# Kernel tuning notes

Hardware: AMD Instinct MI355X
Metric: run time of the kernel (lower is better)

## Reference

```python
import jax, jax.numpy as jnp
import numpy as np

B, T, D_MODEL, D_K = 4, 4096, 1024, 64

def setup_inputs() -> dict:
    key = jax.random.key(0)
    k1, k2, k3, k4, k5 = jax.random.split(key, 5)
    x = jax.random.normal(k1, (B, T, D_MODEL), dtype=jnp.float32)
    # rotary freqs_cis as (real, imag) pairs: unit-magnitude like real RoPE
    theta = 10000.0
    inv = 1.0 / (theta ** (jnp.arange(0, D_K, 2, dtype=jnp.float32) / D_K))  # [D_K//2]
    ang = jnp.arange(T, dtype=jnp.float32)[:, None] * inv[None, :]           # [T, D_K//2]
    freqs_cis = jnp.stack([jnp.cos(ang), jnp.sin(ang)], axis=-1)             # [T, D_K//2, 2]
    scale = 1.0 / np.sqrt(D_MODEL)
    Wq = jax.random.normal(k2, (D_MODEL, D_K), dtype=jnp.float32) * scale
    Wk = jax.random.normal(k3, (D_MODEL, D_K), dtype=jnp.float32) * scale
    Wv = jax.random.normal(k4, (D_MODEL, D_K), dtype=jnp.float32) * scale
    return {"x": x, "freqs_cis": freqs_cis, "Wq": Wq, "Wk": Wk, "Wv": Wv}

def _apply_rope(t, fr, fi):
    # t: [B,T,D_K]; fr/fi: [T, D_K//2]. Complex mult on (even, odd) pairs.
    tp = t.reshape(*t.shape[:-1], D_K // 2, 2)       # [B,T,P,2]
    tr, ti = tp[..., 0], tp[..., 1]
    or_ = tr * fr - ti * fi
    oi_ = tr * fi + ti * fr
    return jnp.stack([or_, oi_], axis=-1).reshape(*t.shape[:-1], D_K)

def reference(x, freqs_cis, Wq, Wk, Wv):
    q = x @ Wq                                       # [B,T,D_K]
    k = x @ Wk
    v = x @ Wv
    fr, fi = freqs_cis[..., 0], freqs_cis[..., 1]    # [T, D_K//2]
    q = _apply_rope(q, fr, fi)
    k = _apply_rope(k, fr, fi)
    wei = jnp.einsum('btd,bsd->bts', q, k) * (D_K ** -0.5)   # [B,T,T]
    causal = jnp.tril(jnp.ones((T, T), dtype=bool))
    wei = jnp.where(causal, wei, -jnp.inf)
    wei = jax.nn.softmax(wei, axis=-1)
    return jnp.einsum('bts,bsd->btd', wei, v)        # [B,T,D_K]
```

## Files before the change

### kernel.cpp

```cpp
#include <hip/hip_runtime.h>
#include <hip/hip_bf16.h>

#define BB 4
#define TT 4096
#define DM 1024
#define DK 64
#define NSPLIT 8

using f32x4  = __attribute__((ext_vector_type(4))) float;
using bf16x8 = __attribute__((ext_vector_type(8))) short;

__device__ __forceinline__ short f2bf(float f) {
    __hip_bfloat16 h = __float2bfloat16(f);
    return __builtin_bit_cast(short, h);
}
__device__ __forceinline__ float bf2f(short s) {
    unsigned int u = ((unsigned int)(unsigned short)s) << 16;
    return __builtin_bit_cast(float, u);
}

__global__ __launch_bounds__(256) void wt_kernel(const float* __restrict__ Wq,
                                                 const float* __restrict__ Wk,
                                                 const float* __restrict__ Wv,
                                                 short* __restrict__ Wt) {
    int idx = blockIdx.x * 256 + threadIdx.x;
    if (idx >= 192 * 1024) return;
    int n = idx >> 10;
    int m = idx & 1023;
    const float* W = (n < 64) ? Wq : (n < 128) ? Wk : Wv;
    int c = n & 63;
    Wt[idx] = f2bf(W[m * 64 + c]);
}

__global__ __launch_bounds__(256, 4) void proj_rope(const float* __restrict__ x,
                                                    const float* __restrict__ freqs,
                                                    const short* __restrict__ Wt,
                                                    short* __restrict__ q,
                                                    short* __restrict__ k,
                                                    short* __restrict__ vt)
{
    __shared__ short As[2][4096];
    __shared__ short Bs[2][4096];

    int t  = threadIdx.x;
    int w  = t >> 6;
    int l  = t & 63;
    int lr = l & 15;
    int lg = (l >> 4) & 3;
    int bx = blockIdx.x;
    int mt = (bx & 7) * 32 + (bx >> 3) / 3;
    int nh = (bx >> 3) % 3;
    int m0 = mt * 64;

    int arow = t >> 2;
    int au2  = (t & 3) * 2;
    int aswz = arow & 7;
    const float* gA = x  + (size_t)(m0 + arow) * DM + au2 * 8;
    const short* gB = Wt + (size_t)(nh * 64 + arow) * DM + au2 * 8;

    f32x4 ar[4]; bf16x8 br[2];

#define LOADG(c_) do { int kk = (c_) << 6;                     \
        ar[0] = *(const f32x4*)(gA + kk);                      \
        ar[1] = *(const f32x4*)(gA + kk + 4);                  \
        ar[2] = *(const f32x4*)(gA + kk + 8);                  \
        ar[3] = *(const f32x4*)(gA + kk + 12);                 \
        br[0] = *(const bf16x8*)(gB + kk);                     \
        br[1] = *(const bf16x8*)(gB + kk + 8);                 \
    } while (0)

#define WRITELDS(buf_) do {                                                    \
        int sa = arow * 64;                                                    \
        bf16x8 a0_, a1_;                                                       \
        for (int j_ = 0; j_ < 4; ++j_) {                                       \
            a0_[j_] = f2bf(ar[0][j_]); a0_[4 + j_] = f2bf(ar[1][j_]);          \
            a1_[j_] = f2bf(ar[2][j_]); a1_[4 + j_] = f2bf(ar[3][j_]);          \
        }                                                                      \
        *(bf16x8*)&As[buf_][sa + (((au2    ) ^ aswz) << 3)] = a0_;             \
        *(bf16x8*)&As[buf_][sa + (((au2 + 1) ^ aswz) << 3)] = a1_;             \
        *(bf16x8*)&Bs[buf_][sa + (((au2    ) ^ aswz) << 3)] = br[0];           \
        *(bf16x8*)&Bs[buf_][sa + (((au2 + 1) ^ aswz) << 3)] = br[1];           \
    } while (0)

    f32x4 acc[4];
#pragma unroll
    for (int i = 0; i < 4; ++i) acc[i] = (f32x4){0.f, 0.f, 0.f, 0.f};

    LOADG(0); WRITELDS(0); LOADG(1);
    __syncthreads();

    int cur = 0;
    int r7 = lr & 7;
    int amrow = (w * 16 + lr) * 64;
    for (int ch = 0; ch < 16; ++ch) {
#pragma unroll
        for (int s = 0; s < 2; ++s) {
            int u0 = s * 4 + lg;
            bf16x8 af = *(const bf16x8*)&As[cur][amrow + ((u0 ^ r7) << 3)];
#pragma unroll
            for (int nt = 0; nt < 4; ++nt) {
                bf16x8 bfr = *(const bf16x8*)&Bs[cur][(nt * 16 + lr) * 64 + ((u0 ^ r7) << 3)];
                acc[nt] = __builtin_amdgcn_mfma_f32_16x16x32_bf16(af, bfr, acc[nt], 0, 0, 0);
            }
        }
        if (ch + 1 < 16) {
            WRITELDS(cur ^ 1);
            if (ch + 2 < 16) LOADG(ch + 2);
            __syncthreads();
            cur ^= 1;
        }
    }
#undef LOADG
#undef WRITELDS

    __syncthreads();

    if (nh == 2) {
        short* vs = &Bs[0][0];
#pragma unroll
        for (int r = 0; r < 4; ++r)
#pragma unroll
            for (int nt = 0; nt < 4; ++nt)
                vs[(w * 16 + lg * 4 + r) * 64 + nt * 16 + lr] = f2bf(acc[nt][r]);
        __syncthreads();
        int b   = mt >> 6;
        int tt0 = (mt & 63) * 64;
        int c   = t >> 2;
        int toff = (t & 3) * 16;
        bf16x8 v0, v1;
#pragma unroll
        for (int j = 0; j < 8; ++j) {
            v0[j] = vs[(toff + j) * 64 + c];
            v1[j] = vs[(toff + 8 + j) * 64 + c];
        }
        short* dstv = vt + ((size_t)b * DK + c) * TT + tt0 + toff;
        *(bf16x8*)dstv = v0;
        *(bf16x8*)(dstv + 8) = v1;
    } else {
        short* dst = nh ? k : q;
        float postscale = nh ? 1.0f : 0.125f;
#pragma unroll
        for (int r = 0; r < 4; ++r) {
            int tg = m0 + w * 16 + lg * 4 + r;
            int tt = tg & (TT - 1);
#pragma unroll
            for (int nt = 0; nt < 4; ++nt) {
                int c = nt * 16 + lr;
                float e = acc[nt][r];
                float p = __shfl_xor(e, 1);
                float2 f = ((const float2*)freqs)[(size_t)tt * 32 + (c >> 1)];
                float sgn = (c & 1) ? f.y : -f.y;
                dst[(size_t)tg * DK + c] = f2bf((e * f.x + p * sgn) * postscale);
            }
        }
    }
}

__global__ __launch_bounds__(256, 4) void attn_kernel(const short* __restrict__ q,
                                                      const short* __restrict__ k,
                                                      const short* __restrict__ vt,
                                                      short* __restrict__ po,
                                                      float* __restrict__ ml)
{
    __shared__ short Kb[64][64];
    __shared__ short Vb[64][64];
    __shared__ short pbuf[4][16][72];

    int w  = threadIdx.x >> 6;
    int l  = threadIdx.x & 63;
    int lr = l & 15;
    int lg = l >> 4;
    int b  = blockIdx.y;
    int s  = blockIdx.z;
    int qt = 63 - blockIdx.x;
    int q0 = qt * 64;
    int qrow_wave = q0 + w * 16;

    const short* qB = q  + (size_t)b * TT * DK;
    const short* kB = k  + (size_t)b * TT * DK;
    const short* vB = vt + (size_t)b * DK * TT;

    bf16x8 qf0 = *(const bf16x8*)(qB + (size_t)(qrow_wave + lr) * DK + 8 * lg);
    bf16x8 qf1 = *(const bf16x8*)(qB + (size_t)(qrow_wave + lr) * DK + 32 + 8 * lg);

    f32x4 of[4];
#pragma unroll
    for (int i = 0; i < 4; ++i) of[i] = (f32x4){0.f, 0.f, 0.f, 0.f};
    float m[4], lsum[4];
#pragma unroll
    for (int r = 0; r < 4; ++r) { m[r] = -INFINITY; lsum[r] = 0.f; }

    int nt = (qt >= s) ? ((qt - s + NSPLIT) >> 3) : 0;

    int srow = threadIdx.x >> 2;
    int u0   = (threadIdx.x & 3) * 2;
    int p0s  = ((u0) ^ (srow & 7)) * 8;
    int p1s  = ((u0 + 1) ^ (srow & 7)) * 8;

    bf16x8 kr0, kr1, vr0, vr1;
    short* mypb = &pbuf[w][0][0];

#define ISSUE(tile_) do {                                                        \
        int kv0_ = (tile_) << 6;                                                 \
        const short* gk_ = kB + (size_t)(kv0_ + srow) * DK + (u0 * 8);           \
        const short* gv_ = vB + (size_t)srow * TT + kv0_ + (u0 * 8);             \
        kr0 = *(const bf16x8*)gk_; kr1 = *(const bf16x8*)(gk_ + 8);              \
        vr0 = *(const bf16x8*)gv_; vr1 = *(const bf16x8*)(gv_ + 8);              \
    } while (0)

#define WRITE() do {                                                             \
        *(bf16x8*)&Kb[srow][p0s] = kr0;                                         \
        *(bf16x8*)&Kb[srow][p1s] = kr1;                                         \
        *(bf16x8*)&Vb[srow][p0s] = vr0;                                         \
        *(bf16x8*)&Vb[srow][p1s] = vr1;                                         \
    } while (0)

    if (nt > 0) {
        ISSUE(s); WRITE();
        if (nt > 1) ISSUE(s + NSPLIT);
        __syncthreads();
        for (int i = 0; i < nt; ++i) {
            int kv0 = (s + i * NSPLIT) << 6;

            f32x4 sc[4];
#pragma unroll
            for (int c = 0; c < 4; ++c) sc[c] = (f32x4){0.f, 0.f, 0.f, 0.f};
#pragma unroll
            for (int c = 0; c < 4; ++c) {
                int row = c * 16 + lr;
                bf16x8 kf0 = *(const bf16x8*)&Kb[row][((lg) ^ (row & 7)) * 8];
                bf16x8 kf1 = *(const bf16x8*)&Kb[row][((4 + lg) ^ (row & 7)) * 8];
                sc[c] = __builtin_amdgcn_mfma_f32_16x16x32_bf16(qf0, kf0, sc[c], 0, 0, 0);
                sc[c] = __builtin_amdgcn_mfma_f32_16x16x32_bf16(qf1, kf1, sc[c], 0, 0, 0);
            }

            if (kv0 == q0) {
#pragma unroll
                for (int r = 0; r < 4; ++r) {
                    int qg = qrow_wave + lg * 4 + r;
#pragma unroll
                    for (int c = 0; c < 4; ++c)
                        sc[c][r] = (kv0 + c * 16 + lr <= qg) ? sc[c][r] : -INFINITY;
                }
            }

            float mx[4];
#pragma unroll
            for (int r = 0; r < 4; ++r)
                mx[r] = fmaxf(fmaxf(sc[0][r], sc[1][r]), fmaxf(sc[2][r], sc[3][r]));
            bool needA = (mx[0] > m[0] + 8.f) || (mx[1] > m[1] + 8.f) ||
                         (mx[2] > m[2] + 8.f) || (mx[3] > m[3] + 8.f);
            if (__any(needA)) {
#pragma unroll
                for (int r = 0; r < 4; ++r) {
                    float t2 = mx[r];
                    t2 = fmaxf(t2, __shfl_xor(t2, 1));
                    t2 = fmaxf(t2, __shfl_xor(t2, 2));
                    t2 = fmaxf(t2, __shfl_xor(t2, 4));
                    t2 = fmaxf(t2, __shfl_xor(t2, 8));
                    float mn = fmaxf(m[r], t2);
                    float alpha = __expf(m[r] - mn);
                    m[r] = mn;
                    lsum[r] *= alpha;
#pragma unroll
                    for (int dt = 0; dt < 4; ++dt) of[dt][r] *= alpha;
                }
            }
#pragma unroll
            for (int r = 0; r < 4; ++r) {
                float p0 = __expf(sc[0][r] - m[r]);
                float p1 = __expf(sc[1][r] - m[r]);
                float p2 = __expf(sc[2][r] - m[r]);
                float p3 = __expf(sc[3][r] - m[r]);
                lsum[r] += (p0 + p1) + (p2 + p3);
                int prow = (lg * 4 + r) * 72;
                mypb[prow + lr]      = f2bf(p0);
                mypb[prow + 16 + lr] = f2bf(p1);
                mypb[prow + 32 + lr] = f2bf(p2);
                mypb[prow + 48 + lr] = f2bf(p3);
            }

#pragma unroll
            for (int ks = 0; ks < 2; ++ks) {
                bf16x8 pa = *(const bf16x8*)(mypb + lr * 72 + ks * 32 + 8 * lg);
#pragma unroll
                for (int dt = 0; dt < 4; ++dt) {
                    int row = dt * 16 + lr;
                    bf16x8 vf = *(const bf16x8*)&Vb[row][((ks * 4 + lg) ^ (row & 7)) * 8];
                    of[dt] = __builtin_amdgcn_mfma_f32_16x16x32_bf16(pa, vf, of[dt], 0, 0, 0);
                }
            }

            if (i + 1 < nt) {
                __syncthreads();
                WRITE();
                if (i + 2 < nt) ISSUE(s + (i + 2) * NSPLIT);
                __syncthreads();
            }
        }
    }
#undef ISSUE
#undef WRITE

#pragma unroll
    for (int r = 0; r < 4; ++r) {
        float ps = lsum[r];
        ps += __shfl_xor(ps, 1);
        ps += __shfl_xor(ps, 2);
        ps += __shfl_xor(ps, 4);
        ps += __shfl_xor(ps, 8);
        lsum[r] = ps;
    }

    short* myo  = po + (((size_t)b * 64 + qt) * NSPLIT + s) * 4096;
    float* myml = ml + (((size_t)b * 64 + qt) * NSPLIT + s) * 128;
#pragma unroll
    for (int r = 0; r < 4; ++r) {
        int row = w * 16 + lg * 4 + r;
#pragma unroll
        for (int dt = 0; dt < 4; ++dt) myo[row * 64 + dt * 16 + lr] = f2bf(of[dt][r]);
        if (lr == 0) { myml[row] = m[r]; myml[64 + row] = lsum[r]; }
    }
}

__global__ __launch_bounds__(256) void merge_kernel(const short* __restrict__ po,
                                                    const float* __restrict__ ml,
                                                    float* __restrict__ out)
{
    int qt = blockIdx.x;
    int b  = blockIdx.y;
    int row = threadIdx.x >> 2;
    int cg  = threadIdx.x & 3;

    size_t mlbase = ((size_t)b * 64 + qt) * NSPLIT * 128;
    float mm[NSPLIT], llv[NSPLIT];
#pragma unroll
    for (int s = 0; s < NSPLIT; ++s) {
        mm[s]  = ml[mlbase + s * 128 + row];
        llv[s] = ml[mlbase + s * 128 + 64 + row];
    }
    float M = -INFINITY;
#pragma unroll
    for (int s = 0; s < NSPLIT; ++s) M = fmaxf(M, mm[s]);
    float e[NSPLIT], den = 0.f;
#pragma unroll
    for (int s = 0; s < NSPLIT; ++s) { e[s] = __expf(mm[s] - M); den += e[s] * llv[s]; }
    float inv = 1.0f / den;

    size_t pbase = ((size_t)b * 64 + qt) * NSPLIT * 4096;
#pragma unroll
    for (int j = 0; j < 2; ++j) {
        int col = cg * 16 + j * 8;
        float acc8[8];
#pragma unroll
        for (int e2 = 0; e2 < 8; ++e2) acc8[e2] = 0.f;
#pragma unroll
        for (int s = 0; s < NSPLIT; ++s) {
            bf16x8 v = *(const bf16x8*)(po + pbase + s * 4096 + row * 64 + col);
#pragma unroll
            for (int e2 = 0; e2 < 8; ++e2) acc8[e2] += e[s] * bf2f(v[e2]);
        }
        float* orow = out + ((size_t)b * TT + qt * 64 + row) * DK + col;
#pragma unroll
        for (int e2 = 0; e2 < 8; ++e2) orow[e2] = acc8[e2] * inv;
    }
}

extern "C" void kernel_launch(void* const* d_in, const int* in_sizes, int n_in,
                              void* d_out, int out_size, void* d_ws, size_t ws_size,
                              hipStream_t stream) {
    const float* x     = (const float*)d_in[0];
    const float* freqs = (const float*)d_in[1];
    const float* Wq    = (const float*)d_in[2];
    const float* Wk    = (const float*)d_in[3];
    const float* Wv    = (const float*)d_in[4];
    float* out = (float*)d_out;

    char* ws = (char*)d_ws;
    short* Wt  = (short*)ws;
    short* qb  = (short*)(ws + 393216);
    short* kb  = (short*)(ws + 2490368);
    short* vtb = (short*)(ws + 4587520);
    short* po  = (short*)(ws + 6684672);
    float* ml  = (float*)(ws + 23461888);

    hipLaunchKernelGGL(wt_kernel, dim3(768), dim3(256), 0, stream, Wq, Wk, Wv, Wt);
    hipLaunchKernelGGL(proj_rope, dim3(768), dim3(256), 0, stream, x, freqs, Wt, qb, kb, vtb);
    hipLaunchKernelGGL(attn_kernel, dim3(64, BB, NSPLIT), dim3(256), 0, stream, qb, kb, vtb, po, ml);
    hipLaunchKernelGGL(merge_kernel, dim3(64, BB), dim3(256), 0, stream, po, ml, out);
}
```

Measured before the change: 66.27 us.

## Load K/V fragments directly from global and remap grid for XCD-local L2 reuse

Removes the shared-memory K/V staging, its double-buffered prefetch and both per-tile __syncthreads, so each wave now loads its MFMA K and V fragments straight from global memory into registers. The grid becomes a flat 2048-block launch whose index is remapped so that each XCD serves a single batch, keeping that batch's K/V working set in one XCD's L2. In exchange, every wave re-reads the same K/V tile from cache (four times the global/L2 traffic per block), and the explicit load-ahead prefetch is gone, which may expose memory latency.

```diff
diff --git a/kernel.cpp b/kernel.cpp
--- a/kernel.cpp
+++ b/kernel.cpp
@@ -162,17 +162,21 @@
                                                       short* __restrict__ po,
                                                       float* __restrict__ ml)
 {
-    __shared__ short Kb[64][64];
-    __shared__ short Vb[64][64];
     __shared__ short pbuf[4][16][72];
 
     int w  = threadIdx.x >> 6;
     int l  = threadIdx.x & 63;
     int lr = l & 15;
     int lg = l >> 4;
-    int b  = blockIdx.y;
-    int s  = blockIdx.z;
-    int qt = 63 - blockIdx.x;
+
+    int wg   = blockIdx.x;
+    int xcd  = wg & 7;
+    int j    = wg >> 3;
+    int b    = xcd >> 1;
+    int p2   = xcd & 1;
+    int idx2 = p2 * 256 + j;
+    int qt   = 63 - ((idx2 >> 3) * 2 + p2) % 64;
+    int s    = idx2 & 7;
     int q0 = qt * 64;
     int qrow_wave = q0 + w * 16;
 
@@ -191,116 +195,89 @@
     for (int r = 0; r < 4; ++r) { m[r] = -INFINITY; lsum[r] = 0.f; }
 
     int nt = (qt >= s) ? ((qt - s + NSPLIT) >> 3) : 0;
-
-    int srow = threadIdx.x >> 2;
-    int u0   = (threadIdx.x & 3) * 2;
-    int p0s  = ((u0) ^ (srow & 7)) * 8;
-    int p1s  = ((u0 + 1) ^ (srow & 7)) * 8;
-
-    bf16x8 kr0, kr1, vr0, vr1;
     short* mypb = &pbuf[w][0][0];
 
-#define ISSUE(tile_) do {                                                        \
-        int kv0_ = (tile_) << 6;                                                 \
-        const short* gk_ = kB + (size_t)(kv0_ + srow) * DK + (u0 * 8);           \
-        const short* gv_ = vB + (size_t)srow * TT + kv0_ + (u0 * 8);             \
-        kr0 = *(const bf16x8*)gk_; kr1 = *(const bf16x8*)(gk_ + 8);              \
-        vr0 = *(const bf16x8*)gv_; vr1 = *(const bf16x8*)(gv_ + 8);              \
-    } while (0)
-
-#define WRITE() do {                                                             \
-        *(bf16x8*)&Kb[srow][p0s] = kr0;                                         \
-        *(bf16x8*)&Kb[srow][p1s] = kr1;                                         \
-        *(bf16x8*)&Vb[srow][p0s] = vr0;                                         \
-        *(bf16x8*)&Vb[srow][p1s] = vr1;                                         \
-    } while (0)
-
-    if (nt > 0) {
-        ISSUE(s); WRITE();
-        if (nt > 1) ISSUE(s + NSPLIT);
-        __syncthreads();
-        for (int i = 0; i < nt; ++i) {
-            int kv0 = (s + i * NSPLIT) << 6;
-
-            f32x4 sc[4];
-#pragma unroll
-            for (int c = 0; c < 4; ++c) sc[c] = (f32x4){0.f, 0.f, 0.f, 0.f};
-#pragma unroll
-            for (int c = 0; c < 4; ++c) {
-                int row = c * 16 + lr;
-                bf16x8 kf0 = *(const bf16x8*)&Kb[row][((lg) ^ (row & 7)) * 8];
-                bf16x8 kf1 = *(const bf16x8*)&Kb[row][((4 + lg) ^ (row & 7)) * 8];
-                sc[c] = __builtin_amdgcn_mfma_f32_16x16x32_bf16(qf0, kf0, sc[c], 0, 0, 0);
-                sc[c] = __builtin_amdgcn_mfma_f32_16x16x32_bf16(qf1, kf1, sc[c], 0, 0, 0);
+    for (int i = 0; i < nt; ++i) {
+        int kv0 = (s + i * NSPLIT) << 6;
+        const short* kT = kB + (size_t)kv0 * DK;
+
+        bf16x8 kf0[4], kf1[4];
+#pragma unroll
+        for (int c = 0; c < 4; ++c) {
+            const short* kr = kT + (size_t)(c * 16 + lr) * DK + 8 * lg;
+            kf0[c] = *(const bf16x8*)kr;
+            kf1[c] = *(const bf16x8*)(kr + 32);
+        }
+        f32x4 sc[4];
+#pragma unroll
+        for (int c = 0; c < 4; ++c) {
+            sc[c] = (f32x4){0.f, 0.f, 0.f, 0.f};
+            sc[c] = __builtin_amdgcn_mfma_f32_16x16x32_bf16(qf0, kf0[c], sc[c], 0, 0, 0);
+            sc[c] = __builtin_amdgcn_mfma_f32_16x16x32_bf16(qf1, kf1[c], sc[c], 0, 0, 0);
+        }
+
+        bf16x8 vf[8];
+#pragma unroll
+        for (int dt = 0; dt < 4; ++dt) {
+            const short* vr = vB + (size_t)(dt * 16 + lr) * TT + kv0 + 8 * lg;
+            vf[dt]     = *(const bf16x8*)vr;
+            vf[4 + dt] = *(const bf16x8*)(vr + 32);
+        }
+
+        if (kv0 == q0) {
+#pragma unroll
+            for (int r = 0; r < 4; ++r) {
+                int qg = qrow_wave + lg * 4 + r;
+#pragma unroll
+                for (int c = 0; c < 4; ++c)
+                    sc[c][r] = (kv0 + c * 16 + lr <= qg) ? sc[c][r] : -INFINITY;
             }
-
-            if (kv0 == q0) {
-#pragma unroll
-                for (int r = 0; r < 4; ++r) {
-                    int qg = qrow_wave + lg * 4 + r;
-#pragma unroll
-                    for (int c = 0; c < 4; ++c)
-                        sc[c][r] = (kv0 + c * 16 + lr <= qg) ? sc[c][r] : -INFINITY;
-                }
+        }
+
+        float mx[4];
+#pragma unroll
+        for (int r = 0; r < 4; ++r)
+            mx[r] = fmaxf(fmaxf(sc[0][r], sc[1][r]), fmaxf(sc[2][r], sc[3][r]));
+        bool needA = (mx[0] > m[0] + 8.f) || (mx[1] > m[1] + 8.f) ||
+                     (mx[2] > m[2] + 8.f) || (mx[3] > m[3] + 8.f);
+        if (__any(needA)) {
+#pragma unroll
+            for (int r = 0; r < 4; ++r) {
+                float t2 = mx[r];
+                t2 = fmaxf(t2, __shfl_xor(t2, 1));
+                t2 = fmaxf(t2, __shfl_xor(t2, 2));
+                t2 = fmaxf(t2, __shfl_xor(t2, 4));
+                t2 = fmaxf(t2, __shfl_xor(t2, 8));
+                float mn = fmaxf(m[r], t2);
+                float alpha = __expf(m[r] - mn);
+                m[r] = mn;
+                lsum[r] *= alpha;
+#pragma unroll
+                for (int dt = 0; dt < 4; ++dt) of[dt][r] *= alpha;
             }
-
-            float mx[4];
-#pragma unroll
-            for (int r = 0; r < 4; ++r)
-                mx[r] = fmaxf(fmaxf(sc[0][r], sc[1][r]), fmaxf(sc[2][r], sc[3][r]));
-            bool needA = (mx[0] > m[0] + 8.f) || (mx[1] > m[1] + 8.f) ||
-                         (mx[2] > m[2] + 8.f) || (mx[3] > m[3] + 8.f);
-            if (__any(needA)) {
-#pragma unroll
-                for (int r = 0; r < 4; ++r) {
-                    float t2 = mx[r];
-                    t2 = fmaxf(t2, __shfl_xor(t2, 1));
-                    t2 = fmaxf(t2, __shfl_xor(t2, 2));
-                    t2 = fmaxf(t2, __shfl_xor(t2, 4));
-                    t2 = fmaxf(t2, __shfl_xor(t2, 8));
-                    float mn = fmaxf(m[r], t2);
-                    float alpha = __expf(m[r] - mn);
-                    m[r] = mn;
-                    lsum[r] *= alpha;
-#pragma unroll
-                    for (int dt = 0; dt < 4; ++dt) of[dt][r] *= alpha;
-                }
-            }
-#pragma unroll
-            for (int r = 0; r < 4; ++r) {
-                float p0 = __expf(sc[0][r] - m[r]);
-                float p1 = __expf(sc[1][r] - m[r]);
-                float p2 = __expf(sc[2][r] - m[r]);
-                float p3 = __expf(sc[3][r] - m[r]);
-                lsum[r] += (p0 + p1) + (p2 + p3);
-                int prow = (lg * 4 + r) * 72;
-                mypb[prow + lr]      = f2bf(p0);
-                mypb[prow + 16 + lr] = f2bf(p1);
-                mypb[prow + 32 + lr] = f2bf(p2);
-                mypb[prow + 48 + lr] = f2bf(p3);
-            }
-
-#pragma unroll
-            for (int ks = 0; ks < 2; ++ks) {
-                bf16x8 pa = *(const bf16x8*)(mypb + lr * 72 + ks * 32 + 8 * lg);
-#pragma unroll
-                for (int dt = 0; dt < 4; ++dt) {
-                    int row = dt * 16 + lr;
-                    bf16x8 vf = *(const bf16x8*)&Vb[row][((ks * 4 + lg) ^ (row & 7)) * 8];
-                    of[dt] = __builtin_amdgcn_mfma_f32_16x16x32_bf16(pa, vf, of[dt], 0, 0, 0);
-                }
-            }
-
-            if (i + 1 < nt) {
-                __syncthreads();
-                WRITE();
-                if (i + 2 < nt) ISSUE(s + (i + 2) * NSPLIT);
-                __syncthreads();
-            }
-        }
-    }
-#undef ISSUE
-#undef WRITE
+        }
+#pragma unroll
+        for (int r = 0; r < 4; ++r) {
+            float p0 = __expf(sc[0][r] - m[r]);
+            float p1 = __expf(sc[1][r] - m[r]);
+            float p2e = __expf(sc[2][r] - m[r]);
+            float p3 = __expf(sc[3][r] - m[r]);
+            lsum[r] += (p0 + p1) + (p2e + p3);
+            int prow = (lg * 4 + r) * 72;
+            mypb[prow + lr]      = f2bf(p0);
+            mypb[prow + 16 + lr] = f2bf(p1);
+            mypb[prow + 32 + lr] = f2bf(p2e);
+            mypb[prow + 48 + lr] = f2bf(p3);
+        }
+
+#pragma unroll
+        for (int ks = 0; ks < 2; ++ks) {
+            bf16x8 pa = *(const bf16x8*)(mypb + lr * 72 + ks * 32 + 8 * lg);
+#pragma unroll
+            for (int dt = 0; dt < 4; ++dt)
+                of[dt] = __builtin_amdgcn_mfma_f32_16x16x32_bf16(pa, vf[ks * 4 + dt], of[dt], 0, 0, 0);
+        }
+    }
 
 #pragma unroll
     for (int r = 0; r < 4; ++r) {
@@ -349,8 +326,8 @@
 
     size_t pbase = ((size_t)b * 64 + qt) * NSPLIT * 4096;
 #pragma unroll
-    for (int j = 0; j < 2; ++j) {
-        int col = cg * 16 + j * 8;
+    for (int jj = 0; jj < 2; ++jj) {
+        int col = cg * 16 + jj * 8;
         float acc8[8];
 #pragma unroll
         for (int e2 = 0; e2 < 8; ++e2) acc8[e2] = 0.f;
@@ -386,6 +363,6 @@
 
     hipLaunchKernelGGL(wt_kernel, dim3(768), dim3(256), 0, stream, Wq, Wk, Wv, Wt);
     hipLaunchKernelGGL(proj_rope, dim3(768), dim3(256), 0, stream, x, freqs, Wt, qb, kb, vtb);
-    hipLaunchKernelGGL(attn_kernel, dim3(64, BB, NSPLIT), dim3(256), 0, stream, qb, kb, vtb, po, ml);
+    hipLaunchKernelGGL(attn_kernel, dim3(2048), dim3(256), 0, stream, qb, kb, vtb, po, ml);
     hipLaunchKernelGGL(merge_kernel, dim3(64, BB), dim3(256), 0, stream, po, ml, out);
 }
```

Result: slower. 104.7 us, median of 2 (+58.1%).

## Process two 64-row query tiles per attention block to reuse staged K/V

Applied to the files above, without the earlier changes.

Each attention block now handles 128 query rows as two 64-row groups, reusing every K/V tile loaded into shared memory for both groups. This halves global-to-LDS K/V traffic and the synchronisation per unit of work, and halves the grid. The cost is higher register pressure from doubled accumulators and query fragments, which can lower occupancy. It also means fewer blocks overall, with a causal imbalance where the first group skips the diagonal-plus-one tile.

```diff
diff --git a/kernel.cpp b/kernel.cpp
--- a/kernel.cpp
+++ b/kernel.cpp
@@ -172,25 +172,33 @@
     int lg = l >> 4;
     int b  = blockIdx.y;
     int s  = blockIdx.z;
-    int qt = 63 - blockIdx.x;
-    int q0 = qt * 64;
-    int qrow_wave = q0 + w * 16;
+    int qt = 31 - blockIdx.x;
+    int q0 = qt * 128;
 
     const short* qB = q  + (size_t)b * TT * DK;
     const short* kB = k  + (size_t)b * TT * DK;
     const short* vB = vt + (size_t)b * DK * TT;
 
-    bf16x8 qf0 = *(const bf16x8*)(qB + (size_t)(qrow_wave + lr) * DK + 8 * lg);
-    bf16x8 qf1 = *(const bf16x8*)(qB + (size_t)(qrow_wave + lr) * DK + 32 + 8 * lg);
-
-    f32x4 of[4];
-#pragma unroll
-    for (int i = 0; i < 4; ++i) of[i] = (f32x4){0.f, 0.f, 0.f, 0.f};
-    float m[4], lsum[4];
-#pragma unroll
-    for (int r = 0; r < 4; ++r) { m[r] = -INFINITY; lsum[r] = 0.f; }
-
-    int nt = (qt >= s) ? ((qt - s + NSPLIT) >> 3) : 0;
+    bf16x8 qf[2][2];
+#pragma unroll
+    for (int rg = 0; rg < 2; ++rg) {
+        int qrow = q0 + rg * 64 + w * 16;
+        qf[rg][0] = *(const bf16x8*)(qB + (size_t)(qrow + lr) * DK + 8 * lg);
+        qf[rg][1] = *(const bf16x8*)(qB + (size_t)(qrow + lr) * DK + 32 + 8 * lg);
+    }
+
+    f32x4 of[2][4];
+    float m[2][4], lsum[2][4];
+#pragma unroll
+    for (int rg = 0; rg < 2; ++rg)
+#pragma unroll
+        for (int r = 0; r < 4; ++r) {
+            of[rg][r] = (f32x4){0.f, 0.f, 0.f, 0.f};
+            m[rg][r] = -INFINITY; lsum[rg][r] = 0.f;
+        }
+
+    int ntot = 2 * qt + 2;
+    int nt   = (s < ntot) ? (((ntot - 1 - s) >> 3) + 1) : 0;
 
     int srow = threadIdx.x >> 2;
     int u0   = (threadIdx.x & 3) * 2;
@@ -222,72 +230,80 @@
         for (int i = 0; i < nt; ++i) {
             int kv0 = (s + i * NSPLIT) << 6;
 
-            f32x4 sc[4];
-#pragma unroll
-            for (int c = 0; c < 4; ++c) sc[c] = (f32x4){0.f, 0.f, 0.f, 0.f};
-#pragma unroll
-            for (int c = 0; c < 4; ++c) {
-                int row = c * 16 + lr;
-                bf16x8 kf0 = *(const bf16x8*)&Kb[row][((lg) ^ (row & 7)) * 8];
-                bf16x8 kf1 = *(const bf16x8*)&Kb[row][((4 + lg) ^ (row & 7)) * 8];
-                sc[c] = __builtin_amdgcn_mfma_f32_16x16x32_bf16(qf0, kf0, sc[c], 0, 0, 0);
-                sc[c] = __builtin_amdgcn_mfma_f32_16x16x32_bf16(qf1, kf1, sc[c], 0, 0, 0);
-            }
-
-            if (kv0 == q0) {
-#pragma unroll
-                for (int r = 0; r < 4; ++r) {
-                    int qg = qrow_wave + lg * 4 + r;
-#pragma unroll
-                    for (int c = 0; c < 4; ++c)
-                        sc[c][r] = (kv0 + c * 16 + lr <= qg) ? sc[c][r] : -INFINITY;
-                }
-            }
-
-            float mx[4];
-#pragma unroll
-            for (int r = 0; r < 4; ++r)
-                mx[r] = fmaxf(fmaxf(sc[0][r], sc[1][r]), fmaxf(sc[2][r], sc[3][r]));
-            bool needA = (mx[0] > m[0] + 8.f) || (mx[1] > m[1] + 8.f) ||
-                         (mx[2] > m[2] + 8.f) || (mx[3] > m[3] + 8.f);
-            if (__any(needA)) {
-#pragma unroll
-                for (int r = 0; r < 4; ++r) {
-                    float t2 = mx[r];
-                    t2 = fmaxf(t2, __shfl_xor(t2, 1));
-                    t2 = fmaxf(t2, __shfl_xor(t2, 2));
-                    t2 = fmaxf(t2, __shfl_xor(t2, 4));
-                    t2 = fmaxf(t2, __shfl_xor(t2, 8));
-                    float mn = fmaxf(m[r], t2);
-                    float alpha = __expf(m[r] - mn);
-                    m[r] = mn;
-                    lsum[r] *= alpha;
-#pragma unroll
-                    for (int dt = 0; dt < 4; ++dt) of[dt][r] *= alpha;
-                }
-            }
-#pragma unroll
-            for (int r = 0; r < 4; ++r) {
-                float p0 = __expf(sc[0][r] - m[r]);
-                float p1 = __expf(sc[1][r] - m[r]);
-                float p2 = __expf(sc[2][r] - m[r]);
-                float p3 = __expf(sc[3][r] - m[r]);
-                lsum[r] += (p0 + p1) + (p2 + p3);
-                int prow = (lg * 4 + r) * 72;
-                mypb[prow + lr]      = f2bf(p0);
-                mypb[prow + 16 + lr] = f2bf(p1);
-                mypb[prow + 32 + lr] = f2bf(p2);
-                mypb[prow + 48 + lr] = f2bf(p3);
-            }
-
-#pragma unroll
-            for (int ks = 0; ks < 2; ++ks) {
-                bf16x8 pa = *(const bf16x8*)(mypb + lr * 72 + ks * 32 + 8 * lg);
-#pragma unroll
-                for (int dt = 0; dt < 4; ++dt) {
-                    int row = dt * 16 + lr;
-                    bf16x8 vf = *(const bf16x8*)&Vb[row][((ks * 4 + lg) ^ (row & 7)) * 8];
-                    of[dt] = __builtin_amdgcn_mfma_f32_16x16x32_bf16(pa, vf, of[dt], 0, 0, 0);
+#pragma unroll
+            for (int rg = 0; rg < 2; ++rg) {
+                int qbase = q0 + rg * 64;
+                if (kv0 <= qbase) {
+                    int qrow_wave = qbase + w * 16;
+
+                    f32x4 sc[4];
+#pragma unroll
+                    for (int c = 0; c < 4; ++c) sc[c] = (f32x4){0.f, 0.f, 0.f, 0.f};
+#pragma unroll
+                    for (int c = 0; c < 4; ++c) {
+                        int row = c * 16 + lr;
+                        bf16x8 kf0 = *(const bf16x8*)&Kb[row][((lg) ^ (row & 7)) * 8];
+                        bf16x8 kf1 = *(const bf16x8*)&Kb[row][((4 + lg) ^ (row & 7)) * 8];
+                        sc[c] = __builtin_amdgcn_mfma_f32_16x16x32_bf16(qf[rg][0], kf0, sc[c], 0, 0, 0);
+                        sc[c] = __builtin_amdgcn_mfma_f32_16x16x32_bf16(qf[rg][1], kf1, sc[c], 0, 0, 0);
+                    }
+
+                    if (kv0 == qbase) {
+#pragma unroll
+                        for (int r = 0; r < 4; ++r) {
+                            int qg = qrow_wave + lg * 4 + r;
+#pragma unroll
+                            for (int c = 0; c < 4; ++c)
+                                sc[c][r] = (kv0 + c * 16 + lr <= qg) ? sc[c][r] : -INFINITY;
+                        }
+                    }
+
+                    float mx[4];
+#pragma unroll
+                    for (int r = 0; r < 4; ++r)
+                        mx[r] = fmaxf(fmaxf(sc[0][r], sc[1][r]), fmaxf(sc[2][r], sc[3][r]));
+                    bool needA = (mx[0] > m[rg][0] + 8.f) || (mx[1] > m[rg][1] + 8.f) ||
+                                 (mx[2] > m[rg][2] + 8.f) || (mx[3] > m[rg][3] + 8.f);
+                    if (__any(needA)) {
+#pragma unroll
+                        for (int r = 0; r < 4; ++r) {
+                            float t2 = mx[r];
+                            t2 = fmaxf(t2, __shfl_xor(t2, 1));
+                            t2 = fmaxf(t2, __shfl_xor(t2, 2));
+                            t2 = fmaxf(t2, __shfl_xor(t2, 4));
+                            t2 = fmaxf(t2, __shfl_xor(t2, 8));
+                            float mn = fmaxf(m[rg][r], t2);
+                            float alpha = __expf(m[rg][r] - mn);
+                            m[rg][r] = mn;
+                            lsum[rg][r] *= alpha;
+#pragma unroll
+                            for (int dt = 0; dt < 4; ++dt) of[rg][dt][r] *= alpha;
+                        }
+                    }
+#pragma unroll
+                    for (int r = 0; r < 4; ++r) {
+                        float p0 = __expf(sc[0][r] - m[rg][r]);
+                        float p1 = __expf(sc[1][r] - m[rg][r]);
+                        float p2 = __expf(sc[2][r] - m[rg][r]);
+                        float p3 = __expf(sc[3][r] - m[rg][r]);
+                        lsum[rg][r] += (p0 + p1) + (p2 + p3);
+                        int prow = (lg * 4 + r) * 72;
+                        mypb[prow + lr]      = f2bf(p0);
+                        mypb[prow + 16 + lr] = f2bf(p1);
+                        mypb[prow + 32 + lr] = f2bf(p2);
+                        mypb[prow + 48 + lr] = f2bf(p3);
+                    }
+
+#pragma unroll
+                    for (int ks = 0; ks < 2; ++ks) {
+                        bf16x8 pa = *(const bf16x8*)(mypb + lr * 72 + ks * 32 + 8 * lg);
+#pragma unroll
+                        for (int dt = 0; dt < 4; ++dt) {
+                            int row = dt * 16 + lr;
+                            bf16x8 vf = *(const bf16x8*)&Vb[row][((ks * 4 + lg) ^ (row & 7)) * 8];
+                            of[rg][dt] = __builtin_amdgcn_mfma_f32_16x16x32_bf16(pa, vf, of[rg][dt], 0, 0, 0);
+                        }
+                    }
                 }
             }
 
@@ -303,23 +319,26 @@
 #undef WRITE
 
 #pragma unroll
-    for (int r = 0; r < 4; ++r) {
-        float ps = lsum[r];
-        ps += __shfl_xor(ps, 1);
-        ps += __shfl_xor(ps, 2);
-        ps += __shfl_xor(ps, 4);
-        ps += __shfl_xor(ps, 8);
-        lsum[r] = ps;
-    }
-
-    short* myo  = po + (((size_t)b * 64 + qt) * NSPLIT + s) * 4096;
-    float* myml = ml + (((size_t)b * 64 + qt) * NSPLIT + s) * 128;
-#pragma unroll
-    for (int r = 0; r < 4; ++r) {
-        int row = w * 16 + lg * 4 + r;
-#pragma unroll
-        for (int dt = 0; dt < 4; ++dt) myo[row * 64 + dt * 16 + lr] = f2bf(of[dt][r]);
-        if (lr == 0) { myml[row] = m[r]; myml[64 + row] = lsum[r]; }
+    for (int rg = 0; rg < 2; ++rg) {
+#pragma unroll
+        for (int r = 0; r < 4; ++r) {
+            float ps = lsum[rg][r];
+            ps += __shfl_xor(ps, 1);
+            ps += __shfl_xor(ps, 2);
+            ps += __shfl_xor(ps, 4);
+            ps += __shfl_xor(ps, 8);
+            lsum[rg][r] = ps;
+        }
+        int qt64 = qt * 2 + rg;
+        short* myo  = po + (((size_t)b * 64 + qt64) * NSPLIT + s) * 4096;
+        float* myml = ml + (((size_t)b * 64 + qt64) * NSPLIT + s) * 128;
+#pragma unroll
+        for (int r = 0; r < 4; ++r) {
+            int row = w * 16 + lg * 4 + r;
+#pragma unroll
+            for (int dt = 0; dt < 4; ++dt) myo[row * 64 + dt * 16 + lr] = f2bf(of[rg][dt][r]);
+            if (lr == 0) { myml[row] = m[rg][r]; myml[64 + row] = lsum[rg][r]; }
+        }
     }
 }
 
@@ -349,8 +368,8 @@
 
     size_t pbase = ((size_t)b * 64 + qt) * NSPLIT * 4096;
 #pragma unroll
-    for (int j = 0; j < 2; ++j) {
-        int col = cg * 16 + j * 8;
+    for (int jj = 0; jj < 2; ++jj) {
+        int col = cg * 16 + jj * 8;
         float acc8[8];
 #pragma unroll
         for (int e2 = 0; e2 < 8; ++e2) acc8[e2] = 0.f;
@@ -386,6 +405,6 @@
 
     hipLaunchKernelGGL(wt_kernel, dim3(768), dim3(256), 0, stream, Wq, Wk, Wv, Wt);
     hipLaunchKernelGGL(proj_rope, dim3(768), dim3(256), 0, stream, x, freqs, Wt, qb, kb, vtb);
-    hipLaunchKernelGGL(attn_kernel, dim3(64, BB, NSPLIT), dim3(256), 0, stream, qb, kb, vtb, po, ml);
+    hipLaunchKernelGGL(attn_kernel, dim3(32, BB, NSPLIT), dim3(256), 0, stream, qb, kb, vtb, po, ml);
     hipLaunchKernelGGL(merge_kernel, dim3(64, BB), dim3(256), 0, stream, po, ml, out);
 }
```

Result: slower. 70.67 us (+6.6%).
